# Kernel tuning notes

Measured on AMD Instinct MI355X. Metric: run time of the kernel, lower is better.

Reference implementation:

```python
import math
import jax, jax.numpy as jnp
import numpy as np

HEADS = 8
LOG_APPROX_VAR = math.log(0.01)  # self.var = 0.01, non-trainable


def clustering(x, approx_log_var, mu, log_var, log_prior):
    """Faithful port of DisentangledAttention.clustering (mi_estimation=False).
    x: [B,H,L,D]; approx_log_var: [B,H,L]; mu/log_var: [H,C,D]; log_prior: [H,C].
    Returns (cluster_probs [B,H,L,C], kl_loss [B,1,1], div_loss [B])."""
    B, H, L, D = x.shape
    xe = x[:, :, :, None, :]                      # [B,H,L,1,D]
    mue = mu[:, None, :, :]                       # [H,1,C,D]
    alv = approx_log_var[:, :, :, None, None]     # [B,H,L,1,1]
    avar = jnp.exp(alv)
    lv = log_var[:, None, :, :]                   # [H,1,C,D]
    var = jnp.exp(lv)
    logp = jax.nn.log_softmax(log_prior, axis=-1)  # [H,C]

    mse = (xe - mue) ** 2 / var                   # [B,H,L,C,D]
    log_pdf = -0.5 * mse.sum(-1) - D * math.pi - 0.5 * lv.sum(-1)  # [B,H,L,C]
    log_pdf = log_pdf + logp[:, None, :]
    log_probs = jax.nn.log_softmax(log_pdf, axis=-1)
    probs = jnp.exp(log_probs)                    # [B,H,L,C]

    logp_b = logp[None, :, None, :]               # broadcast prior log-probs
    prior = jnp.exp(logp_b)
    # F.kl_div(log_probs, prior) = prior * (log(prior) - log_probs)
    kl = (prior * (logp_b - log_probs)).sum(-1).mean(axis=(1, 2))            # [B]
    kl = kl + 0.5 * (probs * (mse + avar / var + lv).sum(-1)).sum(-1).mean(axis=(1, 2))
    kl = kl - 0.5 * jnp.mean(((1.0 + alv).sum(-1)) * D, axis=(1, 2, 3))
    kl_loss = kl.reshape(-1, 1, 1)

    eyeL = jnp.eye(L, dtype=x.dtype)
    div = jnp.einsum('bhqc,bhkc->bhqk', probs, probs)   # [B,H,L,L]
    div = (div - eyeL) ** 2
    wmask = eyeL * 1.25 + (1.0 - eyeL) * 0.75
    div_loss = (div * wmask).mean(axis=(1, 2, 3))       # [B]
    return probs, kl_loss, div_loss


def setup_inputs() -> dict:
    k = jax.random.key(0)
    ks = jax.random.split(k, 10)
    B, L, D, H, C = 4, 1024, 512, HEADS, 8
    Dk = D // H
    lin_std = 1.0 / math.sqrt(2.0 * D)  # xavier_normal gain=1/sqrt(2)
    return {
        'query': jax.random.normal(ks[0], (B, L, D), jnp.float32),
        'key': jax.random.normal(ks[1], (B, L, D), jnp.float32),
        'value': jax.random.normal(ks[2], (B, L, D), jnp.float32),
        'padding_mask': jnp.zeros((B, 1, L), jnp.float32),
        'Wq': jax.random.normal(ks[3], (D, D), jnp.float32) * lin_std,
        'bq': jnp.zeros((D,), jnp.float32),
        'Wk': jax.random.normal(ks[4], (D, D), jnp.float32) * lin_std,
        'bk': jnp.zeros((D,), jnp.float32),
        'Wv': jax.random.normal(ks[5], (D, D), jnp.float32) * lin_std,
        'bv': jnp.zeros((D,), jnp.float32),
        'Wo': jax.random.normal(ks[6], (D, D), jnp.float32) * lin_std,
        'bo': jnp.zeros((D,), jnp.float32),
        'tok_mu': jax.random.normal(ks[7], (H, C, Dk), jnp.float32) * 0.1,
        'tok_log_var': jnp.zeros((H, C, Dk), jnp.float32),
        'tok_log_prior': jnp.full((H, C), math.log(1.0 / C), jnp.float32),
    }


def reference(query, key, value, padding_mask, Wq, bq, Wk, bk, Wv, bv, Wo, bo,
              tok_mu, tok_log_var, tok_log_prior):
    B, L, D = query.shape
    H = HEADS
    Dk = D // H

    # GMM clustering on raw (unprojected) per-head query/key, eval mode (no reparam noise)
    qh = query.reshape(B, L, H, Dk).transpose(0, 2, 1, 3)  # [B,H,L,Dk]
    kh = key.reshape(B, L, H, Dk).transpose(0, 2, 1, 3)
    alv = jnp.full((B, H, L), LOG_APPROX_VAR, dtype=query.dtype)
    probs_q, kl_q, div_q = clustering(qh, alv, tok_mu, tok_log_var, tok_log_prior)
    probs_k, kl_k, div_k = clustering(kh, alv, tok_mu, tok_log_var, tok_log_prior)

    # Disentangled mask: tokens sharing clusters attend (mask==1 means blocked)
    sim = jnp.einsum('bhqc,bhkc->bhqk', probs_q, probs_k)   # [B,H,L,L]
    cmask = jnp.clip(1.0 - sim + padding_mask[:, :, None, :], 0.0, 1.0)

    # Projections + scaled softmax attention (per softmax_attention/full_attention)
    q = (query @ Wq.T + bq).reshape(B, L, H, Dk).transpose(0, 2, 1, 3) / math.sqrt(Dk)
    kk = (key @ Wk.T + bk).reshape(B, L, H, Dk).transpose(0, 2, 1, 3)
    v = (value @ Wv.T + bv).reshape(B, L, H, Dk).transpose(0, 2, 1, 3)
    scores = jnp.einsum('bhqd,bhkd->bhqk', q, kk) + jax.lax.stop_gradient(cmask) * (-10000.0)
    attn = jax.nn.softmax(scores, axis=-1) * (1.0 - cmask)
    out = jnp.einsum('bhqk,bhkd->bhqd', attn, v).transpose(0, 2, 1, 3).reshape(B, L, D)
    out = out @ Wo.T + bo

    kl_loss = kl_q + kl_k                      # [B,1,1]
    div_loss = (div_q + div_k).reshape(-1, 1, 1)  # [B,1,1]
    return out, kl_loss, div_loss
```

## Files before the change

### kernel.cpp

```cpp
#include <hip/hip_runtime.h>
#include <hip/hip_bf16.h>
#include <math.h>

#define NB 4
#define NL 1024
#define ND 512
#define NH 8
#define NC 8
#define NDK 64

static constexpr float KL3_CONST = 115.36544595161891f;

typedef __bf16 bf16x8 __attribute__((ext_vector_type(8)));
typedef float  f32x4v __attribute__((ext_vector_type(4)));
typedef unsigned short u16x4 __attribute__((ext_vector_type(4)));
typedef unsigned short u16x8 __attribute__((ext_vector_type(8)));

__device__ __forceinline__ unsigned short bf16u(float f) {
    return __builtin_bit_cast(unsigned short, (__bf16)f);
}

struct GemmArgs {
    const void* A; const float* W; const float* bias; void* out;
    float scale; int abf; int obf; int brow; int ostr; int vmap;
};

__device__ __forceinline__ void gemm_body(const GemmArgs& g, unsigned char* smem)
{
    unsigned short* As = (unsigned short*)smem;
    unsigned short* Ws = (unsigned short*)(smem + 10240);
    const int tid = threadIdx.x;
    const int n0 = (g.vmap ? blockIdx.y : blockIdx.x) * 128;
    const int m0 = (g.vmap ? blockIdx.x : blockIdx.y) * 128;

    const int kc = tid & 7;
    const int r0 = tid >> 3;
    const int wave = tid >> 6, lane = tid & 63;
    const int wm = wave >> 1, wn = wave & 1;
    const int r16 = lane & 15, quad = lane >> 4;

    f32x4v acc[4][4];
#pragma unroll
    for (int mi = 0; mi < 4; ++mi)
#pragma unroll
        for (int ni = 0; ni < 4; ++ni)
            acc[mi][ni] = (f32x4v){0.f, 0.f, 0.f, 0.f};

    u16x4 apre[4], wpre[4];
    auto ldA = [&](int k0, int rr) -> u16x4 {
        const int r = r0 + rr * 32;
        if (g.abf) {
            return *(const u16x4*)((const unsigned short*)g.A + (size_t)(m0 + r) * 512 + k0 + kc * 4);
        } else {
            const float4 av = *(const float4*)((const float*)g.A + (size_t)(m0 + r) * 512 + k0 + kc * 4);
            return (u16x4){ bf16u(av.x), bf16u(av.y), bf16u(av.z), bf16u(av.w) };
        }
    };
    auto ldW = [&](int k0, int rr) -> u16x4 {
        const int r = r0 + rr * 32;
        const float4 wv = *(const float4*)(g.W + (size_t)(n0 + r) * 512 + k0 + kc * 4);
        return (u16x4){ bf16u(wv.x), bf16u(wv.y), bf16u(wv.z), bf16u(wv.w) };
    };
#pragma unroll
    for (int rr = 0; rr < 4; ++rr) { apre[rr] = ldA(0, rr); wpre[rr] = ldW(0, rr); }

    for (int k0 = 0; k0 < 512; k0 += 32) {
        __syncthreads();
#pragma unroll
        for (int rr = 0; rr < 4; ++rr) {
            const int r = r0 + rr * 32;
            *(u16x4*)(As + r * 40 + kc * 4) = apre[rr];
            *(u16x4*)(Ws + r * 40 + kc * 4) = wpre[rr];
        }
        __syncthreads();
        if (k0 < 480) {
#pragma unroll
            for (int rr = 0; rr < 4; ++rr) { apre[rr] = ldA(k0 + 32, rr); wpre[rr] = ldW(k0 + 32, rr); }
        }

        bf16x8 af[4], bfr[4];
#pragma unroll
        for (int mi = 0; mi < 4; ++mi)
            af[mi] = *(const bf16x8*)(As + (wm * 64 + mi * 16 + r16) * 40 + quad * 8);
#pragma unroll
        for (int ni = 0; ni < 4; ++ni)
            bfr[ni] = *(const bf16x8*)(Ws + (wn * 64 + ni * 16 + r16) * 40 + quad * 8);
#pragma unroll
        for (int mi = 0; mi < 4; ++mi)
#pragma unroll
            for (int ni = 0; ni < 4; ++ni)
                acc[mi][ni] = __builtin_amdgcn_mfma_f32_16x16x32_bf16(af[mi], bfr[ni], acc[mi][ni], 0, 0, 0);
    }

#pragma unroll
    for (int ni = 0; ni < 4; ++ni) {
        const int col = n0 + wn * 64 + ni * 16 + r16;
        const float bcol = g.brow ? 0.f : g.bias[col];
#pragma unroll
        for (int mi = 0; mi < 4; ++mi) {
#pragma unroll
            for (int i = 0; i < 4; ++i) {
                const int row = m0 + wm * 64 + mi * 16 + quad * 4 + i;
                const float bv = g.brow ? g.bias[row] : bcol;
                const float v = (acc[mi][ni][i] + bv) * g.scale;
                if (g.obf) ((unsigned short*)g.out)[(size_t)row * g.ostr + col] = bf16u(v);
                else       ((float*)g.out)[(size_t)row * g.ostr + col] = v;
            }
        }
    }
}

__device__ __forceinline__ void cluster_body(
    const float* __restrict__ query, const float* __restrict__ key,
    const float* __restrict__ tok_mu, const float* __restrict__ tok_log_var,
    const float* __restrict__ tok_log_prior,
    float* __restrict__ probs_q, float* __restrict__ probs_k,
    float* __restrict__ klp, float* __restrict__ divp, float* __restrict__ Gp,
    unsigned char* smem)
{
    float* mu_s    = (float*)smem;
    float* iv_s    = (float*)(smem + 2048);
    float* Pl      = (float*)(smem + 4096);
    float* Gpart   = (float*)(smem + 13312);
    float* red_s   = (float*)(smem + 14336);
    float* lvsum_s = (float*)(smem + 14368);
    float* alpha_s = (float*)(smem + 14400);
    float* logp_s  = (float*)(smem + 14432);
    float* prior_s = (float*)(smem + 14464);

    const int tid  = threadIdx.x;
    const int bh   = blockIdx.y;
    const int b    = bh >> 3, h = bh & 7;
    const int side = blockIdx.z - 3;
    const int blocklin = side * 128 + bh * 4 + blockIdx.x;
    const float* src = side ? key : query;
    float* probs_out = side ? probs_k : probs_q;

    for (int i = tid; i < 512; i += 256) {
        mu_s[i] = tok_mu[h * 512 + i];
        float lv = tok_log_var[h * 512 + i];
        iv_s[i] = __expf(-lv);
    }
    if (tid < 8) {
        float ls = 0.f, al = 0.f;
        for (int d = 0; d < 64; ++d) {
            float lv = tok_log_var[(h * 8 + tid) * 64 + d];
            ls += lv;
            al += 0.01f * __expf(-lv) + lv;
        }
        lvsum_s[tid] = ls; alpha_s[tid] = al;
    }
    if (tid == 0) {
        float lp[8]; float mx = -1e30f;
        for (int c = 0; c < 8; ++c) { lp[c] = tok_log_prior[h * 8 + c]; mx = fmaxf(mx, lp[c]); }
        float se = 0.f;
        for (int c = 0; c < 8; ++c) se += __expf(lp[c] - mx);
        float lse = mx + __logf(se);
        for (int c = 0; c < 8; ++c) { logp_s[c] = lp[c] - lse; prior_s[c] = __expf(lp[c] - lse); }
    }
    __syncthreads();

    const int l = blockIdx.x * 256 + tid;
    const float4* xp = (const float4*)(src + ((size_t)(b * NL + l)) * ND + h * NDK);
    float4 xr[16];
#pragma unroll
    for (int i = 0; i < 16; ++i) xr[i] = xp[i];

    float ms[8];
#pragma unroll
    for (int c = 0; c < 8; ++c) {
        const float4* mc = (const float4*)(mu_s + c * 64);
        const float4* ic = (const float4*)(iv_s + c * 64);
        float s = 0.f;
#pragma unroll
        for (int i = 0; i < 16; ++i) {
            float4 m4 = mc[i], v4 = ic[i], x4 = xr[i];
            float dx = x4.x - m4.x; s = fmaf(dx * dx, v4.x, s);
            float dy = x4.y - m4.y; s = fmaf(dy * dy, v4.y, s);
            float dz = x4.z - m4.z; s = fmaf(dz * dz, v4.z, s);
            float dw = x4.w - m4.w; s = fmaf(dw * dw, v4.w, s);
        }
        ms[c] = s;
    }

    float lpdf[8]; float mx = -1e30f;
#pragma unroll
    for (int c = 0; c < 8; ++c) {
        lpdf[c] = -0.5f * (ms[c] + lvsum_s[c]) + logp_s[c];
        mx = fmaxf(mx, lpdf[c]);
    }
    float e[8]; float se = 0.f;
#pragma unroll
    for (int c = 0; c < 8; ++c) { e[c] = __expf(lpdf[c] - mx); se += e[c]; }
    float lse = __logf(se);
    float inv = 1.f / se;
    float p[8]; float kl1 = 0.f, kl2 = 0.f, sqq = 0.f;
#pragma unroll
    for (int c = 0; c < 8; ++c) {
        p[c] = e[c] * inv;
        float logprob = lpdf[c] - mx - lse;
        kl1 += prior_s[c] * (logp_s[c] - logprob);
        kl2 += p[c] * (ms[c] + alpha_s[c]);
        sqq = fmaf(p[c], p[c], sqq);
    }

    float* po = probs_out + ((size_t)((b * NH + h) * NL + l)) * NC;
    ((float4*)po)[0] = make_float4(p[0], p[1], p[2], p[3]);
    ((float4*)po)[1] = make_float4(p[4], p[5], p[6], p[7]);
#pragma unroll
    for (int c = 0; c < 8; ++c) Pl[tid * 9 + c] = p[c];

    float dterm = 1.25f * (sqq - 1.f) * (sqq - 1.f) - 0.75f * sqq * sqq;
    float klv = kl1 + 0.5f * kl2;
    __syncthreads();

    {
        int qt = tid >> 6, pos = tid & 63, c1 = pos >> 3, c2 = pos & 7;
        float g = 0.f;
        for (int i = 0; i < 64; ++i) {
            int ll = qt * 64 + i;
            g = fmaf(Pl[ll * 9 + c1], Pl[ll * 9 + c2], g);
        }
        Gpart[qt * 64 + pos] = g;
    }

#pragma unroll
    for (int o = 32; o > 0; o >>= 1) {
        klv   += __shfl_down(klv, o);
        dterm += __shfl_down(dterm, o);
    }
    if ((tid & 63) == 0) { red_s[tid >> 6] = klv; red_s[4 + (tid >> 6)] = dterm; }
    __syncthreads();
    if (tid == 0) {
        klp[blocklin]  = red_s[0] + red_s[1] + red_s[2] + red_s[3];
        divp[blocklin] = red_s[4] + red_s[5] + red_s[6] + red_s[7];
    }
    if (tid < 64)
        Gp[(size_t)blocklin * 64 + tid] =
            Gpart[tid] + Gpart[64 + tid] + Gpart[128 + tid] + Gpart[192 + tid];
}

__global__ __launch_bounds__(256) void fused_front(
    GemmArgs g0, GemmArgs g1, GemmArgs g2,
    const float* query, const float* key,
    const float* tok_mu, const float* tok_log_var, const float* tok_log_prior,
    float* probs_q, float* probs_k,
    float* klp, float* divp, float* Gp)
{
    __shared__ alignas(16) unsigned char smem[20480];
    if (blockIdx.z >= 3) {
        cluster_body(query, key, tok_mu, tok_log_var, tok_log_prior,
                     probs_q, probs_k, klp, divp, Gp, smem);
        return;
    }
    GemmArgs g = (blockIdx.z == 0) ? g0 : ((blockIdx.z == 1) ? g1 : g2);
    gemm_body(g, smem);
}

#define APAD 72

__global__ __launch_bounds__(128) void attn_mfma3_kernel(
    const unsigned short* __restrict__ qp16, const unsigned short* __restrict__ kp16,
    const unsigned short* __restrict__ vtp16,
    const float* __restrict__ probs_q, const float* __restrict__ probs_k,
    const float* __restrict__ padding_mask, unsigned short* __restrict__ ao16)
{
    const int tid = threadIdx.x, lane = tid & 63, w = tid >> 6;
    const int r16 = lane & 15, quad = lane >> 4;
    const int b = blockIdx.z, h = blockIdx.y;
    const int qbase = blockIdx.x * 32;

    __shared__ alignas(16) unsigned short Ks[64 * APAD];
    __shared__ alignas(16) unsigned short Vt[64 * APAD];
    __shared__ alignas(16) unsigned short Ps[2][16 * APAD];
    __shared__ float pk_s[8 * 65];
    __shared__ float pm_s[64];

    bf16x8 qa[2];
    {
        const unsigned short* qrow = qp16 + ((size_t)(b * NL + qbase + w * 16 + r16)) * ND + h * NDK;
        qa[0] = *(const bf16x8*)(qrow + quad * 8);
        qa[1] = *(const bf16x8*)(qrow + 32 + quad * 8);
    }
    float pq[4][8];
#pragma unroll
    for (int i = 0; i < 4; ++i) {
        const float* pr = probs_q + ((size_t)((b * NH + h) * NL + qbase + w * 16 + quad * 4 + i)) * NC;
        float4 a = ((const float4*)pr)[0], c = ((const float4*)pr)[1];
        pq[i][0] = a.x; pq[i][1] = a.y; pq[i][2] = a.z; pq[i][3] = a.w;
        pq[i][4] = c.x; pq[i][5] = c.y; pq[i][6] = c.z; pq[i][7] = c.w;
    }

    f32x4v oacc[4];
#pragma unroll
    for (int n = 0; n < 4; ++n) oacc[n] = (f32x4v){0.f, 0.f, 0.f, 0.f};
    float m_i[4] = {-1e30f, -1e30f, -1e30f, -1e30f};
    float l_i[4] = {0.f, 0.f, 0.f, 0.f};

    for (int kt = 0; kt < 16; ++kt) {
        const int key0 = kt * 64;
        __syncthreads();

#pragma unroll
        for (int i = 0; i < 4; ++i) {
            const int c = i * 128 + tid;
            const int row = c >> 3, c8 = c & 7;
            u16x8 kv = *(const u16x8*)(kp16 + ((size_t)(b * NL + key0 + row)) * ND + h * NDK + c8 * 8);
            *(u16x8*)(Ks + row * APAD + c8 * 8) = kv;
            u16x8 vv = *(const u16x8*)(vtp16 + ((size_t)(h * 64 + row)) * (NB * NL) + b * NL + key0 + c8 * 8);
            *(u16x8*)(Vt + row * APAD + c8 * 8) = vv;
        }
        {
            const int key = tid >> 1, half = tid & 1;
            float4 p = *(const float4*)(probs_k + ((size_t)((b * NH + h) * NL + key0 + key)) * NC + half * 4);
            pk_s[(half * 4 + 0) * 65 + key] = p.x;
            pk_s[(half * 4 + 1) * 65 + key] = p.y;
            pk_s[(half * 4 + 2) * 65 + key] = p.z;
            pk_s[(half * 4 + 3) * 65 + key] = p.w;
        }
        if (tid < 64) pm_s[tid] = padding_mask[b * NL + key0 + tid];
        __syncthreads();

        f32x4v sacc[4];
#pragma unroll
        for (int t = 0; t < 4; ++t) {
            sacc[t] = (f32x4v){0.f, 0.f, 0.f, 0.f};
            bf16x8 kb0 = *(const bf16x8*)(Ks + (t * 16 + r16) * APAD + quad * 8);
            bf16x8 kb1 = *(const bf16x8*)(Ks + (t * 16 + r16) * APAD + 32 + quad * 8);
            sacc[t] = __builtin_amdgcn_mfma_f32_16x16x32_bf16(qa[0], kb0, sacc[t], 0, 0, 0);
            sacc[t] = __builtin_amdgcn_mfma_f32_16x16x32_bf16(qa[1], kb1, sacc[t], 0, 0, 0);
        }

        float sc[4][4], wgt[4][4];
#pragma unroll
        for (int t = 0; t < 4; ++t) {
            const int keyl = t * 16 + r16;
            float pkc[8];
#pragma unroll
            for (int c = 0; c < 8; ++c) pkc[c] = pk_s[c * 65 + keyl];
            const float pmv = pm_s[keyl];
#pragma unroll
            for (int i = 0; i < 4; ++i) {
                float sim = 0.f;
#pragma unroll
                for (int c = 0; c < 8; ++c) sim = fmaf(pq[i][c], pkc[c], sim);
                float cm = 1.f - sim + pmv;
                cm = fminf(fmaxf(cm, 0.f), 1.f);
                sc[t][i] = sacc[t][i] - 10000.f * cm;
                wgt[t][i] = 1.f - cm;
            }
        }

        float mx[4];
#pragma unroll
        for (int i = 0; i < 4; ++i)
            mx[i] = fmaxf(fmaxf(sc[0][i], sc[1][i]), fmaxf(sc[2][i], sc[3][i]));
#pragma unroll
        for (int o = 1; o < 16; o <<= 1) {
#pragma unroll
            for (int i = 0; i < 4; ++i) mx[i] = fmaxf(mx[i], __shfl_xor(mx[i], o));
        }
        float rr[4];
#pragma unroll
        for (int i = 0; i < 4; ++i) {
            const float mnew = fmaxf(m_i[i], mx[i]);
            rr[i] = __expf(m_i[i] - mnew);
            m_i[i] = mnew;
            l_i[i] *= rr[i];
        }
#pragma unroll
        for (int n = 0; n < 4; ++n) {
            oacc[n][0] *= rr[0]; oacc[n][1] *= rr[1];
            oacc[n][2] *= rr[2]; oacc[n][3] *= rr[3];
        }
        float lad[4] = {0.f, 0.f, 0.f, 0.f};
#pragma unroll
        for (int t = 0; t < 4; ++t) {
#pragma unroll
            for (int i = 0; i < 4; ++i) {
                const float p = __expf(sc[t][i] - m_i[i]);
                lad[i] += p;
                Ps[w][(quad * 4 + i) * APAD + t * 16 + r16] = bf16u(p * wgt[t][i]);
            }
        }
#pragma unroll
        for (int o = 1; o < 16; o <<= 1) {
#pragma unroll
            for (int i = 0; i < 4; ++i) lad[i] += __shfl_xor(lad[i], o);
        }
#pragma unroll
        for (int i = 0; i < 4; ++i) l_i[i] += lad[i];

        bf16x8 pa0 = *(const bf16x8*)(Ps[w] + r16 * APAD + quad * 8);
        bf16x8 pa1 = *(const bf16x8*)(Ps[w] + r16 * APAD + 32 + quad * 8);
#pragma unroll
        for (int n = 0; n < 4; ++n) {
            bf16x8 vb0 = *(const bf16x8*)(Vt + (n * 16 + r16) * APAD + quad * 8);
            bf16x8 vb1 = *(const bf16x8*)(Vt + (n * 16 + r16) * APAD + 32 + quad * 8);
            oacc[n] = __builtin_amdgcn_mfma_f32_16x16x32_bf16(pa0, vb0, oacc[n], 0, 0, 0);
            oacc[n] = __builtin_amdgcn_mfma_f32_16x16x32_bf16(pa1, vb1, oacc[n], 0, 0, 0);
        }
    }

#pragma unroll
    for (int i = 0; i < 4; ++i) {
        const float inv = 1.f / l_i[i];
        const int q = qbase + w * 16 + quad * 4 + i;
        unsigned short* orow = ao16 + ((size_t)(b * NL + q)) * ND + h * NDK;
#pragma unroll
        for (int n = 0; n < 4; ++n) orow[n * 16 + r16] = bf16u(oacc[n][i] * inv);
    }
}

__device__ __forceinline__ void finalize_body(
    const float* __restrict__ klp, const float* __restrict__ divp,
    const float* __restrict__ Gp, float* __restrict__ out_tail)
{
    const int tid = threadIdx.x, b = tid >> 6, lane = tid & 63;
    float gsum = 0.f;
#pragma unroll
    for (int s = 0; s < 2; ++s)
#pragma unroll
        for (int h = 0; h < 8; ++h) {
            const int base = s * 128 + (b * 8 + h) * 4;
            float Ge = 0.f;
#pragma unroll
            for (int x = 0; x < 4; ++x) Ge += Gp[(size_t)(base + x) * 64 + lane];
            gsum = fmaf(Ge, Ge, gsum);
        }
    const int s = lane >> 5, rem = lane & 31, h = rem >> 2, x = rem & 3;
    const int idx = s * 128 + (b * 8 + h) * 4 + x;
    float klv = klp[idx];
    float dvv = divp[idx];
#pragma unroll
    for (int o = 32; o > 0; o >>= 1) {
        gsum += __shfl_down(gsum, o);
        klv  += __shfl_down(klv, o);
        dvv  += __shfl_down(dvv, o);
    }
    if (lane == 0) {
        out_tail[b]     = klv * (1.0f / 8192.0f) + 2.0f * KL3_CONST;
        out_tail[4 + b] = (dvv + 0.75f * gsum) * (1.0f / 8388608.0f);
    }
}

__global__ __launch_bounds__(256) void fused_back(
    GemmArgs g0,
    const float* klp, const float* divp, const float* Gp, float* out_tail)
{
    __shared__ alignas(16) unsigned char smem[20480];
    if (blockIdx.z == 1) {
        if (blockIdx.x == 0 && blockIdx.y == 0)
            finalize_body(klp, divp, Gp, out_tail);
        return;
    }
    gemm_body(g0, smem);
}

extern "C" void kernel_launch(void* const* d_in, const int* in_sizes, int n_in,
                              void* d_out, int out_size, void* d_ws, size_t ws_size,
                              hipStream_t stream)
{
    const float* query        = (const float*)d_in[0];
    const float* key          = (const float*)d_in[1];
    const float* value        = (const float*)d_in[2];
    const float* padding_mask = (const float*)d_in[3];
    const float* Wq = (const float*)d_in[4];
    const float* bq = (const float*)d_in[5];
    const float* Wk = (const float*)d_in[6];
    const float* bk = (const float*)d_in[7];
    const float* Wv = (const float*)d_in[8];
    const float* bv = (const float*)d_in[9];
    const float* Wo = (const float*)d_in[10];
    const float* bo = (const float*)d_in[11];
    const float* tok_mu        = (const float*)d_in[12];
    const float* tok_log_var   = (const float*)d_in[13];
    const float* tok_log_prior = (const float*)d_in[14];

    float* ws = (float*)d_ws;
    const size_t FS = 1048576;
    unsigned short* qp16  = (unsigned short*)ws;
    unsigned short* kp16  = (unsigned short*)(ws + FS);
    unsigned short* vtp16 = (unsigned short*)(ws + 2 * FS);
    unsigned short* ao16  = (unsigned short*)(ws + 3 * FS);
    float* probs_q = ws + 4 * FS;
    float* probs_k = probs_q + (size_t)NB * NH * NL * NC;
    float* klp     = probs_k + (size_t)NB * NH * NL * NC;
    float* divp    = klp + 256;
    float* Gp      = divp + 256;

    GemmArgs gq {query, Wq, bq, qp16, 0.125f, 0, 1, 0, 512, 0};
    GemmArgs gk {key,   Wk, bk, kp16, 1.f,    0, 1, 0, 512, 0};
    GemmArgs gvt{Wv, value, bv, vtp16, 1.f,   0, 1, 1, 4096, 1};
    fused_front<<<dim3(4, 32, 5), 256, 0, stream>>>(
        gq, gk, gvt, query, key, tok_mu, tok_log_var, tok_log_prior,
        probs_q, probs_k, klp, divp, Gp);

    attn_mfma3_kernel<<<dim3(32, NH, NB), 128, 0, stream>>>(
        qp16, kp16, vtp16, probs_q, probs_k, padding_mask, ao16);

    GemmArgs go{ao16, Wo, bo, d_out, 1.f, 1, 0, 0, 512, 0};
    fused_back<<<dim3(4, 32, 2), 256, 0, stream>>>(
        go, klp, divp, Gp, (float*)d_out + (size_t)NB * NL * ND);
}
```

Before: 211.6 us.

## Split attention over key halves with merge pass and use 64-row GEMM tiles

Attention now splits each query tile's keys into two halves across separate blocks, doubling the grid. Each block writes unnormalized partial outputs plus row max and sum, and a new merge kernel combines them flash-decoding style into bf16 before the output projection. The GEMM tile changes from 128x128 to 64x128 with a two-stage register prefetch, doubling the number of GEMM blocks, and the cluster blocks are remapped so the front grid still covers everything. The aim is more blocks to fill the GPU's CUs, at the cost of an extra kernel launch and a round trip of fp32 partials through global memory.

```diff
diff --git a/kernel.cpp b/kernel.cpp
--- a/kernel.cpp
+++ b/kernel.cpp
@@ -28,84 +28,87 @@
 __device__ __forceinline__ void gemm_body(const GemmArgs& g, unsigned char* smem)
 {
     unsigned short* As = (unsigned short*)smem;
-    unsigned short* Ws = (unsigned short*)(smem + 10240);
+    unsigned short* Ws = (unsigned short*)(smem + 5120);
     const int tid = threadIdx.x;
-    const int n0 = (g.vmap ? blockIdx.y : blockIdx.x) * 128;
-    const int m0 = (g.vmap ? blockIdx.x : blockIdx.y) * 128;
-
-    const int kc = tid & 7;
-    const int r0 = tid >> 3;
-    const int wave = tid >> 6, lane = tid & 63;
-    const int wm = wave >> 1, wn = wave & 1;
+    int n0, m0;
+    if (g.vmap) {
+        const int linear = blockIdx.y * 4 + blockIdx.x;
+        n0 = (linear & 31) * 128;
+        m0 = (linear >> 5) * 64;
+    } else {
+        n0 = blockIdx.x * 128;
+        m0 = blockIdx.y * 64;
+    }
+
+    const int w = tid >> 6, lane = tid & 63;
     const int r16 = lane & 15, quad = lane >> 4;
-
-    f32x4v acc[4][4];
-#pragma unroll
-    for (int mi = 0; mi < 4; ++mi)
-#pragma unroll
-        for (int ni = 0; ni < 4; ++ni)
-            acc[mi][ni] = (f32x4v){0.f, 0.f, 0.f, 0.f};
-
-    u16x4 apre[4], wpre[4];
-    auto ldA = [&](int k0, int rr) -> u16x4 {
-        const int r = r0 + rr * 32;
+    const int arow = tid >> 2, akc = tid & 3;
+    const int wrow = tid >> 1, wkc = tid & 1;
+
+    f32x4v acc[8];
+#pragma unroll
+    for (int n = 0; n < 8; ++n) acc[n] = (f32x4v){0.f, 0.f, 0.f, 0.f};
+
+    auto ldA = [&](int k0) -> u16x8 {
         if (g.abf) {
-            return *(const u16x4*)((const unsigned short*)g.A + (size_t)(m0 + r) * 512 + k0 + kc * 4);
-        } else {
-            const float4 av = *(const float4*)((const float*)g.A + (size_t)(m0 + r) * 512 + k0 + kc * 4);
-            return (u16x4){ bf16u(av.x), bf16u(av.y), bf16u(av.z), bf16u(av.w) };
-        }
+            return *(const u16x8*)((const unsigned short*)g.A + (size_t)(m0 + arow) * 512 + k0 + akc * 8);
+        }
+        const float* ap = (const float*)g.A + (size_t)(m0 + arow) * 512 + k0 + akc * 8;
+        const float4 a0 = *(const float4*)ap, a1 = *(const float4*)(ap + 4);
+        return (u16x8){ bf16u(a0.x), bf16u(a0.y), bf16u(a0.z), bf16u(a0.w),
+                        bf16u(a1.x), bf16u(a1.y), bf16u(a1.z), bf16u(a1.w) };
     };
-    auto ldW = [&](int k0, int rr) -> u16x4 {
-        const int r = r0 + rr * 32;
-        const float4 wv = *(const float4*)(g.W + (size_t)(n0 + r) * 512 + k0 + kc * 4);
-        return (u16x4){ bf16u(wv.x), bf16u(wv.y), bf16u(wv.z), bf16u(wv.w) };
+    auto ldW = [&](int k0, u16x8* dst) {
+        const float* wp = (const float*)g.W + (size_t)(n0 + wrow) * 512 + k0 + wkc * 16;
+        const float4 w0 = *(const float4*)wp,       w1 = *(const float4*)(wp + 4);
+        const float4 w2 = *(const float4*)(wp + 8), w3 = *(const float4*)(wp + 12);
+        dst[0] = (u16x8){ bf16u(w0.x), bf16u(w0.y), bf16u(w0.z), bf16u(w0.w),
+                          bf16u(w1.x), bf16u(w1.y), bf16u(w1.z), bf16u(w1.w) };
+        dst[1] = (u16x8){ bf16u(w2.x), bf16u(w2.y), bf16u(w2.z), bf16u(w2.w),
+                          bf16u(w3.x), bf16u(w3.y), bf16u(w3.z), bf16u(w3.w) };
     };
-#pragma unroll
-    for (int rr = 0; rr < 4; ++rr) { apre[rr] = ldA(0, rr); wpre[rr] = ldW(0, rr); }
-
-    for (int k0 = 0; k0 < 512; k0 += 32) {
+    auto store_stage = [&](const u16x8& sa, const u16x8* sw) {
+        *(u16x8*)(As + arow * 40 + akc * 8) = sa;
+        *(u16x8*)(Ws + wrow * 40 + wkc * 16) = sw[0];
+        *(u16x8*)(Ws + wrow * 40 + wkc * 16 + 8) = sw[1];
+    };
+    auto mfma_half = [&]() {
+        bf16x8 af = *(const bf16x8*)(As + (w * 16 + r16) * 40 + quad * 8);
+#pragma unroll
+        for (int ni = 0; ni < 8; ++ni) {
+            bf16x8 bfr = *(const bf16x8*)(Ws + (ni * 16 + r16) * 40 + quad * 8);
+            acc[ni] = __builtin_amdgcn_mfma_f32_16x16x32_bf16(af, bfr, acc[ni], 0, 0, 0);
+        }
+    };
+
+    u16x8 sa0 = ldA(0),  sw0[2]; ldW(0, sw0);
+    u16x8 sa1 = ldA(32), sw1[2]; ldW(32, sw1);
+
+    for (int k0 = 0; k0 < 512; k0 += 64) {
         __syncthreads();
-#pragma unroll
-        for (int rr = 0; rr < 4; ++rr) {
-            const int r = r0 + rr * 32;
-            *(u16x4*)(As + r * 40 + kc * 4) = apre[rr];
-            *(u16x4*)(Ws + r * 40 + kc * 4) = wpre[rr];
-        }
+        store_stage(sa0, sw0);
         __syncthreads();
-        if (k0 < 480) {
-#pragma unroll
-            for (int rr = 0; rr < 4; ++rr) { apre[rr] = ldA(k0 + 32, rr); wpre[rr] = ldW(k0 + 32, rr); }
-        }
-
-        bf16x8 af[4], bfr[4];
-#pragma unroll
-        for (int mi = 0; mi < 4; ++mi)
-            af[mi] = *(const bf16x8*)(As + (wm * 64 + mi * 16 + r16) * 40 + quad * 8);
-#pragma unroll
-        for (int ni = 0; ni < 4; ++ni)
-            bfr[ni] = *(const bf16x8*)(Ws + (wn * 64 + ni * 16 + r16) * 40 + quad * 8);
-#pragma unroll
-        for (int mi = 0; mi < 4; ++mi)
-#pragma unroll
-            for (int ni = 0; ni < 4; ++ni)
-                acc[mi][ni] = __builtin_amdgcn_mfma_f32_16x16x32_bf16(af[mi], bfr[ni], acc[mi][ni], 0, 0, 0);
-    }
-
-#pragma unroll
-    for (int ni = 0; ni < 4; ++ni) {
-        const int col = n0 + wn * 64 + ni * 16 + r16;
+        if (k0 + 64 < 512) { sa0 = ldA(k0 + 64); ldW(k0 + 64, sw0); }
+        mfma_half();
+
+        __syncthreads();
+        store_stage(sa1, sw1);
+        __syncthreads();
+        if (k0 + 96 < 512) { sa1 = ldA(k0 + 96); ldW(k0 + 96, sw1); }
+        mfma_half();
+    }
+
+#pragma unroll
+    for (int ni = 0; ni < 8; ++ni) {
+        const int col = n0 + ni * 16 + r16;
         const float bcol = g.brow ? 0.f : g.bias[col];
 #pragma unroll
-        for (int mi = 0; mi < 4; ++mi) {
-#pragma unroll
-            for (int i = 0; i < 4; ++i) {
-                const int row = m0 + wm * 64 + mi * 16 + quad * 4 + i;
-                const float bv = g.brow ? g.bias[row] : bcol;
-                const float v = (acc[mi][ni][i] + bv) * g.scale;
-                if (g.obf) ((unsigned short*)g.out)[(size_t)row * g.ostr + col] = bf16u(v);
-                else       ((float*)g.out)[(size_t)row * g.ostr + col] = v;
-            }
+        for (int i = 0; i < 4; ++i) {
+            const int row = m0 + w * 16 + quad * 4 + i;
+            const float bv = g.brow ? g.bias[row] : bcol;
+            const float v = (acc[ni][i] + bv) * g.scale;
+            if (g.obf) ((unsigned short*)g.out)[(size_t)row * g.ostr + col] = bf16u(v);
+            else       ((float*)g.out)[(size_t)row * g.ostr + col] = v;
         }
     }
 }
@@ -116,7 +119,7 @@
     const float* __restrict__ tok_log_prior,
     float* __restrict__ probs_q, float* __restrict__ probs_k,
     float* __restrict__ klp, float* __restrict__ divp, float* __restrict__ Gp,
-    unsigned char* smem)
+    int linear, unsigned char* smem)
 {
     float* mu_s    = (float*)smem;
     float* iv_s    = (float*)(smem + 2048);
@@ -129,10 +132,11 @@
     float* prior_s = (float*)(smem + 14464);
 
     const int tid  = threadIdx.x;
-    const int bh   = blockIdx.y;
+    const int side = linear >> 7;
+    const int rem  = linear & 127;
+    const int bh   = rem >> 2, chunk = rem & 3;
     const int b    = bh >> 3, h = bh & 7;
-    const int side = blockIdx.z - 3;
-    const int blocklin = side * 128 + bh * 4 + blockIdx.x;
+    const int blocklin = side * 128 + bh * 4 + chunk;
     const float* src = side ? key : query;
     float* probs_out = side ? probs_k : probs_q;
 
@@ -160,7 +164,7 @@
     }
     __syncthreads();
 
-    const int l = blockIdx.x * 256 + tid;
+    const int l = chunk * 256 + tid;
     const float4* xp = (const float4*)(src + ((size_t)(b * NL + l)) * ND + h * NDK);
     float4 xr[16];
 #pragma unroll
@@ -247,10 +251,11 @@
     float* probs_q, float* probs_k,
     float* klp, float* divp, float* Gp)
 {
-    __shared__ alignas(16) unsigned char smem[20480];
-    if (blockIdx.z >= 3) {
+    __shared__ alignas(16) unsigned char smem[15488];
+    if (blockIdx.z == 3) {
+        const int linear = blockIdx.y * 4 + blockIdx.x;
         cluster_body(query, key, tok_mu, tok_log_var, tok_log_prior,
-                     probs_q, probs_k, klp, divp, Gp, smem);
+                     probs_q, probs_k, klp, divp, Gp, linear, smem);
         return;
     }
     GemmArgs g = (blockIdx.z == 0) ? g0 : ((blockIdx.z == 1) ? g1 : g2);
@@ -259,16 +264,20 @@
 
 #define APAD 72
 
-__global__ __launch_bounds__(128) void attn_mfma3_kernel(
+__global__ __launch_bounds__(128) void attn_mfma3s_kernel(
     const unsigned short* __restrict__ qp16, const unsigned short* __restrict__ kp16,
     const unsigned short* __restrict__ vtp16,
     const float* __restrict__ probs_q, const float* __restrict__ probs_k,
-    const float* __restrict__ padding_mask, unsigned short* __restrict__ ao16)
+    const float* __restrict__ padding_mask,
+    float* __restrict__ pO, float* __restrict__ pML)
 {
     const int tid = threadIdx.x, lane = tid & 63, w = tid >> 6;
     const int r16 = lane & 15, quad = lane >> 4;
-    const int b = blockIdx.z, h = blockIdx.y;
-    const int qbase = blockIdx.x * 32;
+    const int b = blockIdx.z >> 1, s = blockIdx.z & 1;
+    const int h = blockIdx.y;
+    const int qt = blockIdx.x;
+    const int qbase = qt * 32;
+    const int sb = ((b * 8 + h) << 5) | qt;
 
     __shared__ alignas(16) unsigned short Ks[64 * APAD];
     __shared__ alignas(16) unsigned short Vt[64 * APAD];
@@ -297,8 +306,8 @@
     float m_i[4] = {-1e30f, -1e30f, -1e30f, -1e30f};
     float l_i[4] = {0.f, 0.f, 0.f, 0.f};
 
-    for (int kt = 0; kt < 16; ++kt) {
-        const int key0 = kt * 64;
+    for (int kt = 0; kt < 8; ++kt) {
+        const int key0 = s * 512 + kt * 64;
         __syncthreads();
 
 #pragma unroll
@@ -402,13 +411,22 @@
         }
     }
 
+    float* po = pO + ((size_t)sb * 2 + s) * 2048;
 #pragma unroll
     for (int i = 0; i < 4; ++i) {
-        const float inv = 1.f / l_i[i];
-        const int q = qbase + w * 16 + quad * 4 + i;
-        unsigned short* orow = ao16 + ((size_t)(b * NL + q)) * ND + h * NDK;
-#pragma unroll
-        for (int n = 0; n < 4; ++n) orow[n * 16 + r16] = bf16u(oacc[n][i] * inv);
+        const int row = w * 16 + quad * 4 + i;
+#pragma unroll
+        for (int n = 0; n < 4; ++n)
+            po[row * 64 + n * 16 + r16] = oacc[n][i];
+    }
+    if (r16 == 0) {
+        float* pml = pML + ((size_t)sb * 2 + s) * 64;
+#pragma unroll
+        for (int i = 0; i < 4; ++i) {
+            const int row = w * 16 + quad * 4 + i;
+            pml[row * 2]     = m_i[i];
+            pml[row * 2 + 1] = l_i[i];
+        }
     }
 }
 
@@ -444,17 +462,42 @@
     }
 }
 
-__global__ __launch_bounds__(256) void fused_back(
-    GemmArgs g0,
-    const float* klp, const float* divp, const float* Gp, float* out_tail)
-{
-    __shared__ alignas(16) unsigned char smem[20480];
-    if (blockIdx.z == 1) {
-        if (blockIdx.x == 0 && blockIdx.y == 0)
-            finalize_body(klp, divp, Gp, out_tail);
-        return;
-    }
-    gemm_body(g0, smem);
+__global__ __launch_bounds__(256) void merge_fin_kernel(
+    const float* __restrict__ pO, const float* __restrict__ pML,
+    unsigned short* __restrict__ ao16,
+    const float* __restrict__ klp, const float* __restrict__ divp,
+    const float* __restrict__ Gp, float* __restrict__ out_tail)
+{
+    if (blockIdx.x == 1024) { finalize_body(klp, divp, Gp, out_tail); return; }
+    const int gid = blockIdx.x * 256 + threadIdx.x;
+    const int sb = gid >> 8, rem = gid & 255;
+    const int row = rem >> 3, d0 = (rem & 7) * 8;
+
+    const float2 ml0 = *(const float2*)(pML + ((size_t)sb * 2 + 0) * 64 + row * 2);
+    const float2 ml1 = *(const float2*)(pML + ((size_t)sb * 2 + 1) * 64 + row * 2);
+    const float M = fmaxf(ml0.x, ml1.x);
+    const float e0 = __expf(ml0.x - M), e1 = __expf(ml1.x - M);
+    const float inv = 1.f / fmaf(ml0.y, e0, ml1.y * e1);
+    const float f0 = e0 * inv, f1 = e1 * inv;
+
+    const float* p0 = pO + ((size_t)sb * 2 + 0) * 2048 + row * 64 + d0;
+    const float* p1 = pO + ((size_t)sb * 2 + 1) * 2048 + row * 64 + d0;
+    const int qt = sb & 31, bh = sb >> 5, h = bh & 7, b = bh >> 3;
+    unsigned short* orow = ao16 + ((size_t)(b * NL + qt * 32 + row)) * ND + h * NDK + d0;
+
+    const float4 a0 = *(const float4*)p0,       a1 = *(const float4*)(p0 + 4);
+    const float4 c0 = *(const float4*)p1,       c1 = *(const float4*)(p1 + 4);
+    u16x8 ov = { bf16u(a0.x * f0 + c0.x * f1), bf16u(a0.y * f0 + c0.y * f1),
+                 bf16u(a0.z * f0 + c0.z * f1), bf16u(a0.w * f0 + c0.w * f1),
+                 bf16u(a1.x * f0 + c1.x * f1), bf16u(a1.y * f0 + c1.y * f1),
+                 bf16u(a1.z * f0 + c1.z * f1), bf16u(a1.w * f0 + c1.w * f1) };
+    *(u16x8*)orow = ov;
+}
+
+__global__ __launch_bounds__(256) void gemm_single(GemmArgs g)
+{
+    __shared__ alignas(16) unsigned char smem[15488];
+    gemm_body(g, smem);
 }
 
 extern "C" void kernel_launch(void* const* d_in, const int* in_sizes, int n_in,
@@ -485,21 +528,25 @@
     unsigned short* ao16  = (unsigned short*)(ws + 3 * FS);
     float* probs_q = ws + 4 * FS;
     float* probs_k = probs_q + (size_t)NB * NH * NL * NC;
-    float* klp     = probs_k + (size_t)NB * NH * NL * NC;
+    float* pO      = probs_k + (size_t)NB * NH * NL * NC;
+    float* pML     = pO + 4194304;
+    float* klp     = pML + 131072;
     float* divp    = klp + 256;
     float* Gp      = divp + 256;
 
     GemmArgs gq {query, Wq, bq, qp16, 0.125f, 0, 1, 0, 512, 0};
     GemmArgs gk {key,   Wk, bk, kp16, 1.f,    0, 1, 0, 512, 0};
     GemmArgs gvt{Wv, value, bv, vtp16, 1.f,   0, 1, 1, 4096, 1};
-    fused_front<<<dim3(4, 32, 5), 256, 0, stream>>>(
+    fused_front<<<dim3(4, 64, 4), 256, 0, stream>>>(
         gq, gk, gvt, query, key, tok_mu, tok_log_var, tok_log_prior,
         probs_q, probs_k, klp, divp, Gp);
 
-    attn_mfma3_kernel<<<dim3(32, NH, NB), 128, 0, stream>>>(
-        qp16, kp16, vtp16, probs_q, probs_k, padding_mask, ao16);
+    attn_mfma3s_kernel<<<dim3(32, NH, NB * 2), 128, 0, stream>>>(
+        qp16, kp16, vtp16, probs_q, probs_k, padding_mask, pO, pML);
+
+    merge_fin_kernel<<<1025, 256, 0, stream>>>(
+        pO, pML, ao16, klp, divp, Gp, (float*)d_out + (size_t)NB * NL * ND);
 
     GemmArgs go{ao16, Wo, bo, d_out, 1.f, 1, 0, 0, 512, 0};
-    fused_back<<<dim3(4, 32, 2), 256, 0, stream>>>(
-        go, klp, divp, Gp, (float*)d_out + (size_t)NB * NL * ND);
-}
+    gemm_single<<<dim3(4, 64, 1), 256, 0, stream>>>(go);
+}
```

After: 211.6 us. Within noise of the previous version (-0.0%).
